# Kernel tuning notes

Measured on AMD Instinct MI355X. Metric: run time of the kernel, lower is better.

The kernel has to match this reference:

```python
import jax, jax.numpy as jnp
import numpy as np

B, T, N, D = 4, 8, 512, 512
K, dh = 8, 64  # D == K * dh
EMB = 64
EPS = 1e-5


def _layernorm(x, g, b):
    mu = jnp.mean(x, axis=-1, keepdims=True)
    var = jnp.mean(jnp.square(x - mu), axis=-1, keepdims=True)
    return (x - mu) * jax.lax.rsqrt(var + EPS) * g + b


def setup_inputs() -> dict:
    key = jax.random.key(0)
    ks = jax.random.split(key, 16)
    s = 1.0 / np.sqrt(D)
    x = jax.random.normal(ks[0], (B, T, N, D), jnp.float32)
    # sparse-ish Laplacian so the adjacency mask (-1e9 where lap==0) is exercised
    lap_dense = jax.random.normal(ks[1], (N, N), jnp.float32)
    keep = jax.random.uniform(ks[2], (N, N)) < 0.1
    lapmatrix = jnp.where(keep, lap_dense, 0.0)
    node_embeddings = jax.random.normal(ks[3], (N, EMB), jnp.float32)
    inp = {
        "x": x,
        "lapmatrix": lapmatrix,
        "node_embeddings": node_embeddings,
        "Wq": jax.random.normal(ks[4], (D, D), jnp.float32) * s,
        "bq": jnp.zeros((D,), jnp.float32),
        "Wk": jax.random.normal(ks[5], (D, D), jnp.float32) * s,
        "bk": jnp.zeros((D,), jnp.float32),
        "Wv": jax.random.normal(ks[6], (D, D), jnp.float32) * s,
        "bv": jnp.zeros((D,), jnp.float32),
        "ln1_g": jnp.ones((D,), jnp.float32),
        "ln1_b": jnp.zeros((D,), jnp.float32),
        "ln2_g": jnp.ones((D,), jnp.float32),
        "ln2_b": jnp.zeros((D,), jnp.float32),
        "alpha": jnp.float32(1.0),
        "beta": jnp.float32(1.0),
        "Wo": jax.random.normal(ks[7], (D, D), jnp.float32) * s,
        "bo": jnp.zeros((D,), jnp.float32),
        "W1": jax.random.normal(ks[8], (4 * D, D), jnp.float32) * s,
        "b1": jnp.zeros((4 * D,), jnp.float32),
        "W2": jax.random.normal(ks[9], (D, 4 * D), jnp.float32) * (1.0 / np.sqrt(4 * D)),
        "b2": jnp.zeros((D,), jnp.float32),
        "k": 3,
    }
    return inp


def reference(x, lapmatrix, node_embeddings, Wq, bq, Wk, bk, Wv, bv,
              ln1_g, ln1_b, ln2_g, ln2_b, alpha, beta, Wo, bo,
              W1, b1, W2, b2, k):
    # k is an unused forward arg in the original module; dropout is eval-mode identity.
    b_, t_, n_, d_ = x.shape
    xn = _layernorm(x, ln1_g, ln1_b)
    q = xn @ Wq.T + bq  # [B,T,N,D]
    ky = xn @ Wk.T + bk
    v = xn @ Wv.T + bv
    # [B,T,N,K,dh] -> [B,T,K,N,dh]
    q = q.reshape(b_, t_, n_, K, dh).transpose(0, 1, 3, 2, 4)
    ky = ky.reshape(b_, t_, n_, K, dh).transpose(0, 1, 3, 2, 4)
    v = v.reshape(b_, t_, n_, K, dh).transpose(0, 1, 3, 2, 4)
    raw = jnp.einsum('btkne,btkme->btknm', q, ky) / jnp.sqrt(jnp.float32(dh))
    # graph biases (broadcast [N,N] over B,T,K instead of materializing expands)
    supports = jax.nn.softmax(jax.nn.relu(node_embeddings @ node_embeddings.T), axis=1)
    mask = jnp.where(lapmatrix != 0, 0.0, -1e9).astype(x.dtype)
    logits = raw + alpha * supports + beta * lapmatrix + mask
    attn = jax.nn.softmax(logits, axis=-1)
    out = jnp.einsum('btknm,btkme->btkne', attn, v)
    out = out.transpose(0, 1, 3, 2, 4).reshape(b_, t_, n_, d_)
    x1 = x + (out @ Wo.T + bo)
    h = jax.nn.relu(_layernorm(x1, ln2_g, ln2_b) @ W1.T + b1)
    return x1 + (h @ W2.T + b2)
```

## Files before the change

kernel.cpp:

```cpp
#include <hip/hip_runtime.h>

typedef __bf16 bf16x8 __attribute__((ext_vector_type(8)));
typedef unsigned short u16x8 __attribute__((ext_vector_type(8)));
typedef float f32x4 __attribute__((ext_vector_type(4)));
typedef unsigned short u16;

__device__ __forceinline__ float bf2f(u16 u) {
    union { unsigned int i; float f; } x; x.i = ((unsigned int)u) << 16; return x.f;
}
__device__ __forceinline__ u16 f2bf(float f) {
    union { float f; unsigned int i; } x; x.f = f;
    unsigned int u = x.i;
    unsigned int r = (u + 0x7FFFu + ((u >> 16) & 1u)) >> 16;
    return (u16)r;
}

#define GL16(g, l) __builtin_amdgcn_global_load_lds( \
    (__attribute__((address_space(1))) void*)(void*)(g), \
    (__attribute__((address_space(3))) void*)(void*)(l), 16, 0, 0)

__global__ __launch_bounds__(256)
void cvt6_kernel(const float* __restrict__ s0, const float* __restrict__ s1,
                 const float* __restrict__ s2, const float* __restrict__ s3,
                 const float* __restrict__ s4, const float* __restrict__ s5,
                 u16* __restrict__ d0, u16* __restrict__ d1, u16* __restrict__ d2,
                 u16* __restrict__ d3, u16* __restrict__ d4, u16* __restrict__ d5)
{
    int b = blockIdx.x;
    const float* s; u16* d; int base;
    if (b < 512) {
        int t = b >> 7, lb = b & 127;
        s = (t == 0) ? s0 : (t == 1) ? s1 : (t == 2) ? s2 : s3;
        d = (t == 0) ? d0 : (t == 1) ? d1 : (t == 2) ? d2 : d3;
        base = lb * 2048;
    } else if (b < 1024) { s = s4; d = d4; base = (b - 512) * 2048; }
    else                 { s = s5; d = d5; base = (b - 1024) * 2048; }
    int i = base + threadIdx.x * 8;
    float4 a = *(const float4*)&s[i];
    float4 c = *(const float4*)&s[i + 4];
    u16x8 o;
    o[0] = f2bf(a.x); o[1] = f2bf(a.y); o[2] = f2bf(a.z); o[3] = f2bf(a.w);
    o[4] = f2bf(c.x); o[5] = f2bf(c.y); o[6] = f2bf(c.z); o[7] = f2bf(c.w);
    *(u16x8*)&d[i] = o;
}

__global__ __launch_bounds__(256)
void bias_kernel(const float* __restrict__ E, const float* __restrict__ lap,
                 const float* __restrict__ alpha_p, const float* __restrict__ beta_p,
                 float* __restrict__ biasout)
{
    __shared__ float wred[8];
    int tid = threadIdx.x;
    int i = blockIdx.x;
    int lane = tid & 63, wave = tid >> 6;
    int j0 = tid, j1 = tid + 256;
    float s0 = 0.f, s1 = 0.f;
#pragma unroll
    for (int t4 = 0; t4 < 16; ++t4) {
        float4 a  = *(const float4*)&E[i * 64 + t4 * 4];
        float4 e0 = *(const float4*)&E[j0 * 64 + t4 * 4];
        float4 e1 = *(const float4*)&E[j1 * 64 + t4 * 4];
        s0 += a.x * e0.x + a.y * e0.y + a.z * e0.z + a.w * e0.w;
        s1 += a.x * e1.x + a.y * e1.y + a.z * e1.z + a.w * e1.w;
    }
    s0 = fmaxf(s0, 0.f); s1 = fmaxf(s1, 0.f);
    float m = fmaxf(s0, s1);
#pragma unroll
    for (int o = 32; o > 0; o >>= 1) m = fmaxf(m, __shfl_xor(m, o));
    if (lane == 0) wred[wave] = m;
    __syncthreads();
    m = fmaxf(fmaxf(wred[0], wred[1]), fmaxf(wred[2], wred[3]));
    float e0v = __expf(s0 - m), e1v = __expf(s1 - m);
    float sum = e0v + e1v;
#pragma unroll
    for (int o = 32; o > 0; o >>= 1) sum += __shfl_xor(sum, o);
    if (lane == 0) wred[4 + wave] = sum;
    __syncthreads();
    float inv = 1.f / (wred[4] + wred[5] + wred[6] + wred[7]);
    float alpha = alpha_p[0], beta = beta_p[0];
    float lv0 = lap[i * 512 + j0];
    float lv1 = lap[i * 512 + j1];
    biasout[i * 512 + j0] = alpha * (e0v * inv) + beta * lv0 + (lv0 != 0.f ? 0.f : -1e9f);
    biasout[i * 512 + j1] = alpha * (e1v * inv) + beta * lv1 + (lv1 != 0.f ? 0.f : -1e9f);
}

__global__ __launch_bounds__(256)
void ln_kernel(const float* __restrict__ X, const float* __restrict__ G,
               const float* __restrict__ Bb, u16* __restrict__ Y)
{
    int row = blockIdx.x * 4 + (threadIdx.x >> 6);
    int lane = threadIdx.x & 63;
    const float* xr = X + (size_t)row * 512 + lane * 8;
    float4 a = *(const float4*)xr;
    float4 b = *(const float4*)(xr + 4);
    float v[8] = {a.x, a.y, a.z, a.w, b.x, b.y, b.z, b.w};
    float s = 0.f, ss = 0.f;
#pragma unroll
    for (int i = 0; i < 8; i++) { s += v[i]; ss += v[i] * v[i]; }
#pragma unroll
    for (int o = 32; o > 0; o >>= 1) { s += __shfl_xor(s, o); ss += __shfl_xor(ss, o); }
    float mu = s * (1.f / 512.f);
    float var = ss * (1.f / 512.f) - mu * mu;
    float rstd = rsqrtf(var + 1e-5f);
    float4 g0 = *(const float4*)&G[lane * 8];
    float4 g1 = *(const float4*)&G[lane * 8 + 4];
    float4 b0 = *(const float4*)&Bb[lane * 8];
    float4 b1 = *(const float4*)&Bb[lane * 8 + 4];
    float gv[8] = {g0.x, g0.y, g0.z, g0.w, g1.x, g1.y, g1.z, g1.w};
    float bv[8] = {b0.x, b0.y, b0.z, b0.w, b1.x, b1.y, b1.z, b1.w};
    u16x8 out;
#pragma unroll
    for (int i = 0; i < 8; i++) out[i] = f2bf((v[i] - mu) * rstd * gv[i] + bv[i]);
    *(u16x8*)&Y[(size_t)row * 512 + lane * 8] = out;
}

__global__ __launch_bounds__(256)
void gemm_bt(const u16* __restrict__ A, const u16* __restrict__ W,
             const float* __restrict__ bias, const float* __restrict__ resid,
             u16* __restrict__ Cb, float* __restrict__ Cf,
             int M, int Kd, int Nout, int mode)
{
    __shared__ __align__(16) u16 lA[128 * 32];
    __shared__ __align__(16) u16 lB[128 * 32];
    int tid = threadIdx.x;
    int lane = tid & 63, wave = tid >> 6;
    int wm = wave >> 1, wn = wave & 1;
    int bid = blockIdx.y * gridDim.x + blockIdx.x;
    int per = (gridDim.x * gridDim.y) >> 3;
    int lb  = (bid & 7) * per + (bid >> 3);
    int bx = lb % gridDim.x, by = lb / gridDim.x;
    int row0 = by * 128, col0 = bx * 128;
    int rl = lane & 15, kq = lane >> 4;
    f32x4 acc[4][4];
#pragma unroll
    for (int i = 0; i < 4; i++)
#pragma unroll
        for (int j = 0; j < 4; j++) acc[i][j] = (f32x4){0.f, 0.f, 0.f, 0.f};

    int c0 = tid,       sr0 = c0 >> 2, sc0 = (c0 & 3) * 8;
    int c1 = 256 + tid, sr1 = c1 >> 2, sc1 = (c1 & 3) * 8;
    const u16* Abase = A + (size_t)row0 * Kd;
    const u16* Wbase = W + (size_t)col0 * Kd;

    for (int k0 = 0; k0 < Kd; k0 += 32) {
        GL16(Abase + (size_t)sr0 * Kd + k0 + sc0, &lA[c0 * 8]);
        GL16(Abase + (size_t)sr1 * Kd + k0 + sc1, &lA[c1 * 8]);
        GL16(Wbase + (size_t)sr0 * Kd + k0 + sc0, &lB[c0 * 8]);
        GL16(Wbase + (size_t)sr1 * Kd + k0 + sc1, &lB[c1 * 8]);
        __syncthreads();
        bf16x8 af[4], bf[4];
#pragma unroll
        for (int i = 0; i < 4; i++) af[i] = *(const bf16x8*)&lA[(wm * 64 + i * 16 + rl) * 32 + kq * 8];
#pragma unroll
        for (int j = 0; j < 4; j++) bf[j] = *(const bf16x8*)&lB[(wn * 64 + j * 16 + rl) * 32 + kq * 8];
#pragma unroll
        for (int i = 0; i < 4; i++)
#pragma unroll
            for (int j = 0; j < 4; j++)
                acc[i][j] = __builtin_amdgcn_mfma_f32_16x16x32_bf16(af[i], bf[j], acc[i][j], 0, 0, 0);
        __syncthreads();
    }
#pragma unroll
    for (int j = 0; j < 4; j++) {
        int col = col0 + wn * 64 + j * 16 + rl;
        float bsv = bias[col];
#pragma unroll
        for (int i = 0; i < 4; i++) {
            int rbase = row0 + wm * 64 + i * 16 + kq * 4;
#pragma unroll
            for (int r = 0; r < 4; r++) {
                float vo = acc[i][j][r] + bsv;
                size_t idx = (size_t)(rbase + r) * Nout + col;
                if (mode == 2)      Cf[idx] = vo + resid[idx];
                else if (mode == 1) Cb[idx] = f2bf(fmaxf(vo, 0.f));
                else                Cb[idx] = f2bf(vo);
            }
        }
    }
}

__global__ __launch_bounds__(256)
void gemm_qkv(const u16* __restrict__ A,
              const u16* __restrict__ W0, const u16* __restrict__ W1, const u16* __restrict__ W2,
              const float* __restrict__ b0, const float* __restrict__ b1, const float* __restrict__ b2,
              u16* __restrict__ C0, u16* __restrict__ C1, u16* __restrict__ C2)
{
    __shared__ __align__(16) u16 lA[128 * 32];
    __shared__ __align__(16) u16 lB[128 * 32];
    const int Kd = 512, Nout = 512;
    int bid = blockIdx.y * gridDim.x + blockIdx.x;
    int per = (gridDim.x * gridDim.y) >> 3;
    int lb  = (bid & 7) * per + (bid >> 3);
    int rest = lb % 12, by = lb / 12;
    int sel = rest >> 2;
    const u16* W = (sel == 0) ? W0 : (sel == 1) ? W1 : W2;
    const float* bias = (sel == 0) ? b0 : (sel == 1) ? b1 : b2;
    u16* Cb = (sel == 0) ? C0 : (sel == 1) ? C1 : C2;
    int tid = threadIdx.x;
    int lane = tid & 63, wave = tid >> 6;
    int wm = wave >> 1, wn = wave & 1;
    int row0 = by * 128, col0 = (rest & 3) * 128;
    int rl = lane & 15, kq = lane >> 4;
    f32x4 acc[4][4];
#pragma unroll
    for (int i = 0; i < 4; i++)
#pragma unroll
        for (int j = 0; j < 4; j++) acc[i][j] = (f32x4){0.f, 0.f, 0.f, 0.f};
    int c0 = tid,       sr0 = c0 >> 2, sc0 = (c0 & 3) * 8;
    int c1 = 256 + tid, sr1 = c1 >> 2, sc1 = (c1 & 3) * 8;
    const u16* Abase = A + (size_t)row0 * Kd;
    const u16* Wbase = W + (size_t)col0 * Kd;
    for (int k0 = 0; k0 < Kd; k0 += 32) {
        GL16(Abase + (size_t)sr0 * Kd + k0 + sc0, &lA[c0 * 8]);
        GL16(Abase + (size_t)sr1 * Kd + k0 + sc1, &lA[c1 * 8]);
        GL16(Wbase + (size_t)sr0 * Kd + k0 + sc0, &lB[c0 * 8]);
        GL16(Wbase + (size_t)sr1 * Kd + k0 + sc1, &lB[c1 * 8]);
        __syncthreads();
        bf16x8 af[4], bf[4];
#pragma unroll
        for (int i = 0; i < 4; i++) af[i] = *(const bf16x8*)&lA[(wm * 64 + i * 16 + rl) * 32 + kq * 8];
#pragma unroll
        for (int j = 0; j < 4; j++) bf[j] = *(const bf16x8*)&lB[(wn * 64 + j * 16 + rl) * 32 + kq * 8];
#pragma unroll
        for (int i = 0; i < 4; i++)
#pragma unroll
            for (int j = 0; j < 4; j++)
                acc[i][j] = __builtin_amdgcn_mfma_f32_16x16x32_bf16(af[i], bf[j], acc[i][j], 0, 0, 0);
        __syncthreads();
    }
#pragma unroll
    for (int j = 0; j < 4; j++) {
        int col = col0 + wn * 64 + j * 16 + rl;
        float bsv = bias[col];
#pragma unroll
        for (int i = 0; i < 4; i++) {
            int rbase = row0 + wm * 64 + i * 16 + kq * 4;
#pragma unroll
            for (int r = 0; r < 4; r++)
                Cb[(size_t)(rbase + r) * Nout + col] = f2bf(acc[i][j][r] + bsv);
        }
    }
}

__global__ __launch_bounds__(256, 2)
void flash_attn(const u16* __restrict__ Q, const u16* __restrict__ Km,
                const u16* __restrict__ V, const float* __restrict__ biasP,
                u16* __restrict__ O)
{
    __shared__ __align__(16) u16 lQ[128 * 64];
    __shared__ __align__(16) u16 lPK[128 * 136];
    __shared__ __align__(16) unsigned int lVt[64 * 68];
    __shared__ float red[2 * 128];
    __shared__ float m_s[128], l_s[128], alpha_s[128], mnew_s[128];

    int tid = threadIdx.x, lane = tid & 63, wave = tid >> 6;
    int wm = wave >> 1, wn = wave & 1;
    int rl = lane & 15, kq = lane >> 4;
    int qt = blockIdx.x, h = blockIdx.y, bt = blockIdx.z;
    int qg0 = qt * 128;
    size_t hb = (size_t)bt * (512 * 512) + h * 64;
    const u16* Qbase = Q + hb + (size_t)qg0 * 512;
    const u16* Kb0   = Km + hb;
    const u16* Vb0   = V + hb;

#pragma unroll
    for (int rep = 0; rep < 4; ++rep) {
        int c = rep * 256 + tid;
        int qr = c >> 3, d0 = (c & 7) * 8;
        GL16(Qbase + (size_t)qr * 512 + d0, &lQ[c * 8]);
    }
    if (tid < 128) { m_s[tid] = -3.0e38f; l_s[tid] = 0.f; }
    __syncthreads();

    bf16x8 af[4][2];
#pragma unroll
    for (int i = 0; i < 4; i++)
#pragma unroll
        for (int s = 0; s < 2; s++)
            af[i][s] = *(const bf16x8*)&lQ[(wm * 64 + i * 16 + rl) * 64 + s * 32 + kq * 8];

    f32x4 o[4][2];
#pragma unroll
    for (int i = 0; i < 4; i++)
#pragma unroll
        for (int jj = 0; jj < 2; jj++) o[i][jj] = (f32x4){0.f, 0.f, 0.f, 0.f};

    for (int t = 0; t < 4; ++t) {
        int kv0 = t * 128;
        __syncthreads();
        const u16* Kbase = Kb0 + (size_t)kv0 * 512;
#pragma unroll
        for (int rep = 0; rep < 4; ++rep) {
            int c = rep * 256 + tid;
            int kv = c >> 3, d0 = (c & 7) * 8;
            GL16(Kbase + (size_t)kv * 512 + d0, &lPK[c * 8]);
        }
        const u16* Vbase = Vb0 + (size_t)kv0 * 512;
#pragma unroll
        for (int rep = 0; rep < 2; ++rep) {
            int idx = rep * 256 + tid;
            int p = idx & 63, e0 = (idx >> 6) * 8;
            const u16* vp0 = Vbase + (size_t)(2 * p) * 512 + e0;
            u16x8 v0 = *(const u16x8*)vp0;
            u16x8 v1 = *(const u16x8*)(vp0 + 512);
#pragma unroll
            for (int u = 0; u < 8; ++u)
                lVt[(e0 + u) * 68 + p] = (unsigned)v0[u] | ((unsigned)v1[u] << 16);
        }
        __syncthreads();

        f32x4 acc[4][4];
#pragma unroll
        for (int j = 0; j < 4; ++j) {
            bf16x8 bk0 = *(const bf16x8*)&lPK[(wn * 64 + j * 16 + rl) * 64 + kq * 8];
            bf16x8 bk1 = *(const bf16x8*)&lPK[(wn * 64 + j * 16 + rl) * 64 + 32 + kq * 8];
#pragma unroll
            for (int i = 0; i < 4; ++i) {
                acc[i][j] = __builtin_amdgcn_mfma_f32_16x16x32_bf16(af[i][0], bk0,
                            (f32x4){0.f, 0.f, 0.f, 0.f}, 0, 0, 0);
                acc[i][j] = __builtin_amdgcn_mfma_f32_16x16x32_bf16(af[i][1], bk1, acc[i][j], 0, 0, 0);
            }
        }
#pragma unroll
        for (int i = 0; i < 4; ++i)
#pragma unroll
            for (int j = 0; j < 4; ++j) {
                int colg = kv0 + wn * 64 + j * 16 + rl;
                const float* bp = biasP + (size_t)(qg0 + wm * 64 + i * 16 + kq * 4) * 512 + colg;
#pragma unroll
                for (int r = 0; r < 4; ++r)
                    acc[i][j][r] = acc[i][j][r] * 0.125f + bp[(size_t)r * 512];
            }

#pragma unroll
        for (int i = 0; i < 4; ++i) {
            float mx[4];
#pragma unroll
            for (int r = 0; r < 4; ++r) {
                mx[r] = fmaxf(fmaxf(acc[i][0][r], acc[i][1][r]), fmaxf(acc[i][2][r], acc[i][3][r]));
#pragma unroll
                for (int off = 8; off > 0; off >>= 1) mx[r] = fmaxf(mx[r], __shfl_xor(mx[r], off));
            }
            if (rl == 0) {
#pragma unroll
                for (int r = 0; r < 4; ++r)
                    red[wn * 128 + wm * 64 + i * 16 + kq * 4 + r] = mx[r];
            }
        }
        __syncthreads();
        if (tid < 128) {
            float pm = fmaxf(red[tid], red[128 + tid]);
            float mo = m_s[tid];
            float mn = fmaxf(mo, pm);
            m_s[tid] = mn; mnew_s[tid] = mn;
            alpha_s[tid] = __expf(mo - mn);
        }
        __syncthreads();

#pragma unroll
        for (int i = 0; i < 4; ++i) {
            int rb = wm * 64 + i * 16 + kq * 4;
            float mn[4], al[4], sm[4];
#pragma unroll
            for (int r = 0; r < 4; ++r) { mn[r] = mnew_s[rb + r]; al[r] = alpha_s[rb + r]; sm[r] = 0.f; }
#pragma unroll
            for (int j = 0; j < 4; ++j) {
                int col = wn * 64 + j * 16 + rl;
#pragma unroll
                for (int r = 0; r < 4; ++r) {
                    float p = __expf(acc[i][j][r] - mn[r]);
                    sm[r] += p;
                    lPK[(rb + r) * 136 + col] = f2bf(p);
                }
            }
#pragma unroll
            for (int jj = 0; jj < 2; ++jj)
#pragma unroll
                for (int r = 0; r < 4; ++r) o[i][jj][r] *= al[r];
#pragma unroll
            for (int r = 0; r < 4; ++r) {
#pragma unroll
                for (int off = 8; off > 0; off >>= 1) sm[r] += __shfl_xor(sm[r], off);
            }
            if (rl == 0) {
#pragma unroll
                for (int r = 0; r < 4; ++r) red[wn * 128 + rb + r] = sm[r];
            }
        }
        __syncthreads();
        if (tid < 128) l_s[tid] = l_s[tid] * alpha_s[tid] + red[tid] + red[128 + tid];

#pragma unroll
        for (int ks = 0; ks < 4; ++ks) {
            bf16x8 aP[4], bV[2];
#pragma unroll
            for (int i = 0; i < 4; ++i)
                aP[i] = *(const bf16x8*)&lPK[(wm * 64 + i * 16 + rl) * 136 + ks * 32 + kq * 8];
#pragma unroll
            for (int jj = 0; jj < 2; ++jj)
                bV[jj] = *(const bf16x8*)&lVt[(wn * 32 + jj * 16 + rl) * 68 + ks * 16 + kq * 4];
#pragma unroll
            for (int i = 0; i < 4; ++i)
#pragma unroll
                for (int jj = 0; jj < 2; ++jj)
                    o[i][jj] = __builtin_amdgcn_mfma_f32_16x16x32_bf16(aP[i], bV[jj], o[i][jj], 0, 0, 0);
        }
    }
    __syncthreads();

    u16* Ob = O + hb + (size_t)qg0 * 512;
#pragma unroll
    for (int i = 0; i < 4; ++i) {
        int rb = wm * 64 + i * 16 + kq * 4;
        float il[4];
#pragma unroll
        for (int r = 0; r < 4; ++r) il[r] = 1.f / l_s[rb + r];
#pragma unroll
        for (int jj = 0; jj < 2; ++jj) {
            int e = wn * 32 + jj * 16 + rl;
#pragma unroll
            for (int r = 0; r < 4; ++r)
                Ob[(size_t)(rb + r) * 512 + e] = f2bf(o[i][jj][r] * il[r]);
        }
    }
}

extern "C" void kernel_launch(void* const* d_in, const int* in_sizes, int n_in,
                              void* d_out, int out_size, void* d_ws, size_t ws_size,
                              hipStream_t stream)
{
    const float* x     = (const float*)d_in[0];
    const float* lap   = (const float*)d_in[1];
    const float* emb   = (const float*)d_in[2];
    const float* Wq    = (const float*)d_in[3];
    const float* bq    = (const float*)d_in[4];
    const float* Wk    = (const float*)d_in[5];
    const float* bk    = (const float*)d_in[6];
    const float* Wv    = (const float*)d_in[7];
    const float* bvv   = (const float*)d_in[8];
    const float* g1    = (const float*)d_in[9];
    const float* bb1   = (const float*)d_in[10];
    const float* g2    = (const float*)d_in[11];
    const float* bb2   = (const float*)d_in[12];
    const float* alpha = (const float*)d_in[13];
    const float* beta  = (const float*)d_in[14];
    const float* Wo    = (const float*)d_in[15];
    const float* bo    = (const float*)d_in[16];
    const float* W1    = (const float*)d_in[17];
    const float* b1    = (const float*)d_in[18];
    const float* W2    = (const float*)d_in[19];
    const float* b2    = (const float*)d_in[20];
    float* out = (float*)d_out;

    const size_t SZ = (size_t)4 * 8 * 512 * 512;
    char* w = (char*)d_ws;
    float* bias = (float*)w;  w += (size_t)512 * 512 * 4;
    u16* wqb = (u16*)w; w += (size_t)512 * 512 * 2;
    u16* wkb = (u16*)w; w += (size_t)512 * 512 * 2;
    u16* wvb = (u16*)w; w += (size_t)512 * 512 * 2;
    u16* wob = (u16*)w; w += (size_t)512 * 512 * 2;
    u16* w1b = (u16*)w; w += (size_t)2048 * 512 * 2;
    u16* w2b = (u16*)w; w += (size_t)512 * 2048 * 2;
    u16* xnb = (u16*)w; w += SZ * 2;
    u16* qb  = (u16*)w; w += SZ * 2;
    u16* kb  = (u16*)w; w += SZ * 2;
    u16* vb  = (u16*)w; w += SZ * 2;
    u16* hb  = (u16*)w; w += (size_t)16384 * 2048 * 2;
    float* x1 = out;

    const int M = 16384;
    cvt6_kernel<<<1536, 256, 0, stream>>>(Wq, Wk, Wv, Wo, W1, W2,
                                          wqb, wkb, wvb, wob, w1b, w2b);
    bias_kernel<<<512, 256, 0, stream>>>(emb, lap, alpha, beta, bias);
    ln_kernel<<<M / 4, 256, 0, stream>>>(x, g1, bb1, xnb);
    gemm_qkv<<<dim3(12, 128), 256, 0, stream>>>(xnb, wqb, wkb, wvb, bq, bk, bvv, qb, kb, vb);
    flash_attn<<<dim3(4, 8, 32), 256, 0, stream>>>(qb, kb, vb, bias, xnb);
    gemm_bt<<<dim3(4, 128), 256, 0, stream>>>(xnb, wob, bo, x, nullptr, x1, M, 512, 512, 2);
    ln_kernel<<<M / 4, 256, 0, stream>>>(x1, g2, bb2, qb);
    gemm_bt<<<dim3(16, 128), 256, 0, stream>>>(qb, w1b, b1, nullptr, hb, nullptr, M, 512, 2048, 1);
    gemm_bt<<<dim3(4, 128), 256, 0, stream>>>(hb, w2b, b2, x1, nullptr, out, M, 2048, 512, 2);
}
```

Measured before the change: 427.4 us.

## Load GEMM fragments directly from global memory into registers, dropping LDS staging

The dense GEMM kernels (QKV projection, output projection, FFN up and down) no longer stage A and W tiles through shared memory with barriers. Each wave now loads its MFMA fragments straight from global memory into registers, with a one-step register prefetch of the next K slice. This removes the LDS round trip and both __syncthreads per K step. In exchange, data that LDS used to share between waves is now fetched by each wave separately, so global and L2 traffic roughly doubles, and the row-strided 16-byte loads are less coalesced.

```diff
diff --git a/kernel.cpp b/kernel.cpp
--- a/kernel.cpp
+++ b/kernel.cpp
@@ -115,13 +115,11 @@
 }
 
 __global__ __launch_bounds__(256)
-void gemm_bt(const u16* __restrict__ A, const u16* __restrict__ W,
-             const float* __restrict__ bias, const float* __restrict__ resid,
-             u16* __restrict__ Cb, float* __restrict__ Cf,
-             int M, int Kd, int Nout, int mode)
-{
-    __shared__ __align__(16) u16 lA[128 * 32];
-    __shared__ __align__(16) u16 lB[128 * 32];
+void gemm_direct(const u16* __restrict__ A, const u16* __restrict__ W,
+                 const float* __restrict__ bias, const float* __restrict__ resid,
+                 u16* __restrict__ Cb, float* __restrict__ Cf,
+                 int M, int Kd, int Nout, int mode)
+{
     int tid = threadIdx.x;
     int lane = tid & 63, wave = tid >> 6;
     int wm = wave >> 1, wn = wave & 1;
@@ -131,42 +129,53 @@
     int bx = lb % gridDim.x, by = lb / gridDim.x;
     int row0 = by * 128, col0 = bx * 128;
     int rl = lane & 15, kq = lane >> 4;
+
+    const u16* Ap = A + (size_t)(row0 + wm * 64 + rl) * Kd + kq * 8;
+    const u16* Wp = W + (size_t)(col0 + wn * 64 + rl) * Kd + kq * 8;
+    const size_t fstep = (size_t)16 * Kd;
+
     f32x4 acc[4][4];
 #pragma unroll
     for (int i = 0; i < 4; i++)
 #pragma unroll
         for (int j = 0; j < 4; j++) acc[i][j] = (f32x4){0.f, 0.f, 0.f, 0.f};
 
-    int c0 = tid,       sr0 = c0 >> 2, sc0 = (c0 & 3) * 8;
-    int c1 = 256 + tid, sr1 = c1 >> 2, sc1 = (c1 & 3) * 8;
-    const u16* Abase = A + (size_t)row0 * Kd;
-    const u16* Wbase = W + (size_t)col0 * Kd;
-
-    for (int k0 = 0; k0 < Kd; k0 += 32) {
-        GL16(Abase + (size_t)sr0 * Kd + k0 + sc0, &lA[c0 * 8]);
-        GL16(Abase + (size_t)sr1 * Kd + k0 + sc1, &lA[c1 * 8]);
-        GL16(Wbase + (size_t)sr0 * Kd + k0 + sc0, &lB[c0 * 8]);
-        GL16(Wbase + (size_t)sr1 * Kd + k0 + sc1, &lB[c1 * 8]);
-        __syncthreads();
-        bf16x8 af[4], bf[4];
-#pragma unroll
-        for (int i = 0; i < 4; i++) af[i] = *(const bf16x8*)&lA[(wm * 64 + i * 16 + rl) * 32 + kq * 8];
-#pragma unroll
-        for (int j = 0; j < 4; j++) bf[j] = *(const bf16x8*)&lB[(wn * 64 + j * 16 + rl) * 32 + kq * 8];
+    bf16x8 ac[4], bc[4];
+#pragma unroll
+    for (int i = 0; i < 4; i++) ac[i] = *(const bf16x8*)(Ap + i * fstep);
+#pragma unroll
+    for (int j = 0; j < 4; j++) bc[j] = *(const bf16x8*)(Wp + j * fstep);
+
+    for (int k0 = 32; k0 < Kd; k0 += 32) {
+        bf16x8 an[4], bn[4];
+#pragma unroll
+        for (int i = 0; i < 4; i++) an[i] = *(const bf16x8*)(Ap + i * fstep + k0);
+#pragma unroll
+        for (int j = 0; j < 4; j++) bn[j] = *(const bf16x8*)(Wp + j * fstep + k0);
 #pragma unroll
         for (int i = 0; i < 4; i++)
 #pragma unroll
             for (int j = 0; j < 4; j++)
-                acc[i][j] = __builtin_amdgcn_mfma_f32_16x16x32_bf16(af[i], bf[j], acc[i][j], 0, 0, 0);
-        __syncthreads();
-    }
+                acc[i][j] = __builtin_amdgcn_mfma_f32_16x16x32_bf16(ac[i], bc[j], acc[i][j], 0, 0, 0);
+#pragma unroll
+        for (int i = 0; i < 4; i++) ac[i] = an[i];
+#pragma unroll
+        for (int j = 0; j < 4; j++) bc[j] = bn[j];
+    }
+#pragma unroll
+    for (int i = 0; i < 4; i++)
+#pragma unroll
+        for (int j = 0; j < 4; j++)
+            acc[i][j] = __builtin_amdgcn_mfma_f32_16x16x32_bf16(ac[i], bc[j], acc[i][j], 0, 0, 0);
+
+    int kq4 = (lane >> 4) * 4;
 #pragma unroll
     for (int j = 0; j < 4; j++) {
         int col = col0 + wn * 64 + j * 16 + rl;
         float bsv = bias[col];
 #pragma unroll
         for (int i = 0; i < 4; i++) {
-            int rbase = row0 + wm * 64 + i * 16 + kq * 4;
+            int rbase = row0 + wm * 64 + i * 16 + kq4;
 #pragma unroll
             for (int r = 0; r < 4; r++) {
                 float vo = acc[i][j][r] + bsv;
@@ -185,8 +194,6 @@
               const float* __restrict__ b0, const float* __restrict__ b1, const float* __restrict__ b2,
               u16* __restrict__ C0, u16* __restrict__ C1, u16* __restrict__ C2)
 {
-    __shared__ __align__(16) u16 lA[128 * 32];
-    __shared__ __align__(16) u16 lB[128 * 32];
     const int Kd = 512, Nout = 512;
     int bid = blockIdx.y * gridDim.x + blockIdx.x;
     int per = (gridDim.x * gridDim.y) >> 3;
@@ -201,40 +208,53 @@
     int wm = wave >> 1, wn = wave & 1;
     int row0 = by * 128, col0 = (rest & 3) * 128;
     int rl = lane & 15, kq = lane >> 4;
+
+    const u16* Ap = A + (size_t)(row0 + wm * 64 + rl) * Kd + kq * 8;
+    const u16* Wp = W + (size_t)(col0 + wn * 64 + rl) * Kd + kq * 8;
+    const size_t fstep = (size_t)16 * Kd;
+
     f32x4 acc[4][4];
 #pragma unroll
     for (int i = 0; i < 4; i++)
 #pragma unroll
         for (int j = 0; j < 4; j++) acc[i][j] = (f32x4){0.f, 0.f, 0.f, 0.f};
-    int c0 = tid,       sr0 = c0 >> 2, sc0 = (c0 & 3) * 8;
-    int c1 = 256 + tid, sr1 = c1 >> 2, sc1 = (c1 & 3) * 8;
-    const u16* Abase = A + (size_t)row0 * Kd;
-    const u16* Wbase = W + (size_t)col0 * Kd;
-    for (int k0 = 0; k0 < Kd; k0 += 32) {
-        GL16(Abase + (size_t)sr0 * Kd + k0 + sc0, &lA[c0 * 8]);
-        GL16(Abase + (size_t)sr1 * Kd + k0 + sc1, &lA[c1 * 8]);
-        GL16(Wbase + (size_t)sr0 * Kd + k0 + sc0, &lB[c0 * 8]);
-        GL16(Wbase + (size_t)sr1 * Kd + k0 + sc1, &lB[c1 * 8]);
-        __syncthreads();
-        bf16x8 af[4], bf[4];
-#pragma unroll
-        for (int i = 0; i < 4; i++) af[i] = *(const bf16x8*)&lA[(wm * 64 + i * 16 + rl) * 32 + kq * 8];
-#pragma unroll
-        for (int j = 0; j < 4; j++) bf[j] = *(const bf16x8*)&lB[(wn * 64 + j * 16 + rl) * 32 + kq * 8];
+
+    bf16x8 ac[4], bc[4];
+#pragma unroll
+    for (int i = 0; i < 4; i++) ac[i] = *(const bf16x8*)(Ap + i * fstep);
+#pragma unroll
+    for (int j = 0; j < 4; j++) bc[j] = *(const bf16x8*)(Wp + j * fstep);
+
+    for (int k0 = 32; k0 < Kd; k0 += 32) {
+        bf16x8 an[4], bn[4];
+#pragma unroll
+        for (int i = 0; i < 4; i++) an[i] = *(const bf16x8*)(Ap + i * fstep + k0);
+#pragma unroll
+        for (int j = 0; j < 4; j++) bn[j] = *(const bf16x8*)(Wp + j * fstep + k0);
 #pragma unroll
         for (int i = 0; i < 4; i++)
 #pragma unroll
             for (int j = 0; j < 4; j++)
-                acc[i][j] = __builtin_amdgcn_mfma_f32_16x16x32_bf16(af[i], bf[j], acc[i][j], 0, 0, 0);
-        __syncthreads();
-    }
+                acc[i][j] = __builtin_amdgcn_mfma_f32_16x16x32_bf16(ac[i], bc[j], acc[i][j], 0, 0, 0);
+#pragma unroll
+        for (int i = 0; i < 4; i++) ac[i] = an[i];
+#pragma unroll
+        for (int j = 0; j < 4; j++) bc[j] = bn[j];
+    }
+#pragma unroll
+    for (int i = 0; i < 4; i++)
+#pragma unroll
+        for (int j = 0; j < 4; j++)
+            acc[i][j] = __builtin_amdgcn_mfma_f32_16x16x32_bf16(ac[i], bc[j], acc[i][j], 0, 0, 0);
+
+    int kq4 = (lane >> 4) * 4;
 #pragma unroll
     for (int j = 0; j < 4; j++) {
         int col = col0 + wn * 64 + j * 16 + rl;
         float bsv = bias[col];
 #pragma unroll
         for (int i = 0; i < 4; i++) {
-            int rbase = row0 + wm * 64 + i * 16 + kq * 4;
+            int rbase = row0 + wm * 64 + i * 16 + kq4;
 #pragma unroll
             for (int r = 0; r < 4; r++)
                 Cb[(size_t)(rbase + r) * Nout + col] = f2bf(acc[i][j][r] + bsv);
@@ -475,8 +495,8 @@
     ln_kernel<<<M / 4, 256, 0, stream>>>(x, g1, bb1, xnb);
     gemm_qkv<<<dim3(12, 128), 256, 0, stream>>>(xnb, wqb, wkb, wvb, bq, bk, bvv, qb, kb, vb);
     flash_attn<<<dim3(4, 8, 32), 256, 0, stream>>>(qb, kb, vb, bias, xnb);
-    gemm_bt<<<dim3(4, 128), 256, 0, stream>>>(xnb, wob, bo, x, nullptr, x1, M, 512, 512, 2);
+    gemm_direct<<<dim3(4, 128), 256, 0, stream>>>(xnb, wob, bo, x, nullptr, x1, M, 512, 512, 2);
     ln_kernel<<<M / 4, 256, 0, stream>>>(x1, g2, bb2, qb);
-    gemm_bt<<<dim3(16, 128), 256, 0, stream>>>(qb, w1b, b1, nullptr, hb, nullptr, M, 512, 2048, 1);
-    gemm_bt<<<dim3(4, 128), 256, 0, stream>>>(hb, w2b, b2, x1, nullptr, out, M, 2048, 512, 2);
-}
+    gemm_direct<<<dim3(16, 128), 256, 0, stream>>>(qb, w1b, b1, nullptr, hb, nullptr, M, 512, 2048, 1);
+    gemm_direct<<<dim3(4, 128), 256, 0, stream>>>(hb, w2b, b2, x1, nullptr, out, M, 2048, 512, 2);
+}
```

Result: slower. 628.3 us (+47.0%).
